# Kernel tuning notes

Measured on AMD Instinct MI355X. Metric: run time of the kernel, lower is better.

The kernel has to match this reference:

```python
import jax, jax.numpy as jnp
import numpy as np

NODE_IN = 163   # sum of X_MAP category sizes
HIDDEN = 64
N_NODES = 100_000
N_EDGES = 1_600_000
N_GRAPHS = 1024
SLOPE = 0.01    # F.leaky_relu default negative slope


def _linear_init(key, fan_in, fan_out):
    kw, kb = jax.random.split(key)
    bound = 1.0 / np.sqrt(fan_in)
    W = jax.random.uniform(kw, (fan_in, fan_out), jnp.float32, -bound, bound)
    b = jax.random.uniform(kb, (fan_out,), jnp.float32, -bound, bound)
    return W, b


def setup_inputs() -> dict:
    key = jax.random.key(0)
    ks = jax.random.split(key, 8)
    x = jax.random.normal(ks[0], (N_NODES, NODE_IN), jnp.float32)
    edge_index = jax.random.randint(ks[1], (2, N_EDGES), 0, N_NODES)
    batch = jnp.sort(jax.random.randint(ks[2], (N_NODES,), 0, N_GRAPHS))
    W0, b0 = _linear_init(ks[3], NODE_IN, HIDDEN)
    W1, b1 = _linear_init(ks[4], HIDDEN, HIDDEN)
    W2, b2 = _linear_init(ks[5], HIDDEN, HIDDEN)
    fc1_W, fc1_b = _linear_init(ks[6], HIDDEN, HIDDEN)
    fc2_W, fc2_b = _linear_init(ks[7], HIDDEN, 1)
    return {"x": x, "edge_index": edge_index, "batch": batch,
            "W0": W0, "b0": b0, "W1": W1, "b1": b1, "W2": W2, "b2": b2,
            "fc1_W": fc1_W, "fc1_b": fc1_b, "fc2_W": fc2_W, "fc2_b": fc2_b}


def reference(x, edge_index, batch, W0, b0, W1, b1, W2, b2, fc1_W, fc1_b, fc2_W, fc2_b):
    src, dst = edge_index[0], edge_index[1]
    # GCN symmetric norm with self-loops: deg[i] = 1 + in-degree(i)
    deg = jax.ops.segment_sum(jnp.ones(N_EDGES, x.dtype), dst, N_NODES) + 1.0
    dis = jax.lax.rsqrt(deg)               # deg^{-1/2}
    edge_norm = dis[src] * dis[dst]        # [E]
    self_norm = dis * dis                  # deg^{-1} for self-loop term

    def gcn_conv(h, W, b):
        h = h @ W                                   # [N, hidden]
        msg = h[src] * edge_norm[:, None]           # gather + scale, [E, hidden]
        agg = jax.ops.segment_sum(msg, dst, N_NODES)
        agg = agg + h * self_norm[:, None]          # self-loop contribution
        return agg + b

    h = x
    for W, b in ((W0, b0), (W1, b1), (W2, b2)):
        h = jax.nn.leaky_relu(gcn_conv(h, W, b), SLOPE)
        # dropout: eval mode (identity)

    # global_mean_pool over batch segments
    counts = jax.ops.segment_sum(jnp.ones(N_NODES, h.dtype), batch, N_GRAPHS)
    pooled = jax.ops.segment_sum(h, batch, N_GRAPHS) / jnp.maximum(counts, 1.0)[:, None]

    out = jax.nn.leaky_relu(pooled @ fc1_W + fc1_b, SLOPE)
    return (out @ fc2_W + fc2_b).squeeze(-1)       # [N_GRAPHS]
```

## Files before the change

kernel.cpp:

```cpp
#include <hip/hip_runtime.h>

#define NN 100000
#define NE 1600000
#define NG 1024
#define NODE_IN 163
#define SLOPE 0.01f
#define NBUK 391
#define BUKSH 8
#define EPB 8192
#define NBLK ((NE + EPB - 1) / EPB)

typedef short s16x8 __attribute__((ext_vector_type(8)));
typedef float f32x4 __attribute__((ext_vector_type(4)));

__device__ __forceinline__ unsigned short bf16_rne(float x) {
  unsigned u = __float_as_uint(x);
  return (unsigned short)((u + 0x7FFFu + ((u >> 16) & 1u)) >> 16);
}
__device__ __forceinline__ float bf16_f32(unsigned short h) {
  return __uint_as_float(((unsigned)h) << 16);
}

__global__ void k_hist(const int* __restrict__ dst, int* __restrict__ bh, int E) {
  __shared__ int h[NBUK];
  for (int i = threadIdx.x; i < NBUK; i += 256) h[i] = 0;
  __syncthreads();
  int beg = blockIdx.x * EPB, end = min(E, beg + EPB);
  for (int e = beg + threadIdx.x; e < end; e += 256) atomicAdd(&h[dst[e] >> BUKSH], 1);
  __syncthreads();
  for (int i = threadIdx.x; i < NBUK; i += 256) bh[blockIdx.x * NBUK + i] = h[i];
}

__global__ void k_bucket_scan(int* __restrict__ bh, int* __restrict__ btot) {
  __shared__ int s[256];
  int bucket = blockIdx.x, tid = threadIdx.x;
  int v = (tid < NBLK) ? bh[tid * NBUK + bucket] : 0;
  s[tid] = v;
  __syncthreads();
  for (int off = 1; off < 256; off <<= 1) {
    int t = (tid >= off) ? s[tid - off] : 0;
    __syncthreads();
    s[tid] += t;
    __syncthreads();
  }
  if (tid < NBLK) bh[tid * NBUK + bucket] = s[tid] - v;
  if (tid == 255) btot[bucket] = s[255];
}

__global__ void k_btot_scan(const int* __restrict__ btot, int* __restrict__ boffs, int E) {
  __shared__ int s[512];
  int tid = threadIdx.x;
  int v = (tid < NBUK) ? btot[tid] : 0;
  s[tid] = v;
  __syncthreads();
  for (int off = 1; off < 512; off <<= 1) {
    int t = (tid >= off) ? s[tid - off] : 0;
    __syncthreads();
    s[tid] += t;
    __syncthreads();
  }
  if (tid < NBUK) boffs[tid] = s[tid] - v;
  if (tid == 0) boffs[NBUK] = E;
}

__global__ void k_scatter(const int* __restrict__ src, const int* __restrict__ dst,
                          const int* __restrict__ bh, const int* __restrict__ boffs,
                          unsigned* __restrict__ bedge, int E) {
  __shared__ int cur[NBUK];
  for (int i = threadIdx.x; i < NBUK; i += 256)
    cur[i] = boffs[i] + bh[blockIdx.x * NBUK + i];
  __syncthreads();
  int beg = blockIdx.x * EPB, end = min(E, beg + EPB);
  for (int e = beg + threadIdx.x; e < end; e += 256) {
    int d = dst[e];
    int pos = atomicAdd(&cur[d >> BUKSH], 1);
    bedge[pos] = (unsigned)src[e] | ((unsigned)(d & 255) << 17);
  }
}

__global__ void k_b2csr(const unsigned* __restrict__ bedge, const int* __restrict__ boffs,
                        int* __restrict__ offs, float* __restrict__ dis,
                        int* __restrict__ csr, int N) {
  __shared__ int lcnt[256];
  __shared__ int s[256];
  __shared__ int lcur[256];
  int b = blockIdx.x, tid = threadIdx.x;
  int beg = boffs[b], end = boffs[b + 1];
  lcnt[tid] = 0;
  __syncthreads();
  for (int e = beg + tid; e < end; e += 256) atomicAdd(&lcnt[bedge[e] >> 17], 1);
  __syncthreads();
  int v = lcnt[tid];
  s[tid] = v;
  __syncthreads();
  for (int off = 1; off < 256; off <<= 1) {
    int t = (tid >= off) ? s[tid - off] : 0;
    __syncthreads();
    s[tid] += t;
    __syncthreads();
  }
  int o = s[tid] - v;
  int node = (b << BUKSH) + tid;
  if (node <= N) offs[node] = beg + o;
  if (node < N) dis[node] = rsqrtf((float)(v + 1));
  lcur[tid] = o;
  __syncthreads();
  for (int e = beg + tid; e < end; e += 256) {
    unsigned w = bedge[e];
    int p = atomicAdd(&lcur[w >> 17], 1);
    csr[beg + p] = (int)(w & 0x1FFFFu);
  }
}

__global__ void k_wsplit(const float* __restrict__ W, short* __restrict__ hi,
                         short* __restrict__ lo, int K, int KP) {
  int idx = blockIdx.x * 256 + threadIdx.x;
  if (idx >= 64 * KP) return;
  int c = idx / KP, kk = idx - c * KP;
  float v = (kk < K) ? W[(size_t)kk * 64 + c] : 0.f;
  unsigned short h = bf16_rne(v);
  hi[idx] = (short)h;
  lo[idx] = (short)bf16_rne(v - bf16_f32(h));
}

template<int K, int KP>
__launch_bounds__(256)
__global__ void k_gemm(const float* __restrict__ X, const short* __restrict__ Whi,
                       const short* __restrict__ Wlo, const float* __restrict__ disv,
                       unsigned short* __restrict__ Y, int N) {
  constexpr int KC = KP / 32;
  constexpr int PA = 40;
  constexpr int PB = 40;
  __shared__ __align__(16) short sAh[2][128 * PA];
  __shared__ __align__(16) short sAl[2][128 * PA];
  __shared__ __align__(16) short sBh[2][64 * PB];
  __shared__ __align__(16) short sBl[2][64 * PB];

  const int tid = threadIdx.x;
  const int lane = tid & 63, wv = tid >> 6;
  const int l15 = lane & 15, l4 = lane >> 4;
  const int gbase = blockIdx.x << 7;

  const int arow = tid >> 1, akh = (tid & 1) << 4;
  int grow = gbase + arow;
  if (K != KP) grow = min(grow, N - 1);
  const float* xr = X + (size_t)grow * K;
  const int bcol = tid >> 2, bk8 = (tid & 3) << 3;

  float4 ra0, ra1, ra2, ra3;
  s16x8 rbh, rbl;

  auto loadA = [&](int c) {
    if (K != KP && c == KC - 1) {
      ra0 = ra1 = ra2 = ra3 = make_float4(0.f, 0.f, 0.f, 0.f);
      if (akh == 0) { ra0.x = xr[160]; ra0.y = xr[161]; ra0.z = xr[162]; }
    } else {
      const float* p = xr + c * 32 + akh;
      ra0 = *(const float4*)(p);
      ra1 = *(const float4*)(p + 4);
      ra2 = *(const float4*)(p + 8);
      ra3 = *(const float4*)(p + 12);
    }
  };
  auto loadB = [&](int c) {
    const size_t o = (size_t)bcol * KP + c * 32 + bk8;
    rbh = *(const s16x8*)(Whi + o);
    rbl = *(const s16x8*)(Wlo + o);
  };
  auto writeLDS = [&](int b) {
    short hb[16], lb[16];
    float v[16] = {ra0.x, ra0.y, ra0.z, ra0.w, ra1.x, ra1.y, ra1.z, ra1.w,
                   ra2.x, ra2.y, ra2.z, ra2.w, ra3.x, ra3.y, ra3.z, ra3.w};
    #pragma unroll
    for (int j = 0; j < 16; ++j) {
      unsigned short h = bf16_rne(v[j]);
      hb[j] = (short)h;
      lb[j] = (short)bf16_rne(v[j] - bf16_f32(h));
    }
    short* ah = sAh[b] + arow * PA + akh;
    *(s16x8*)(ah) = *(const s16x8*)(hb);
    *(s16x8*)(ah + 8) = *(const s16x8*)(hb + 8);
    short* al = sAl[b] + arow * PA + akh;
    *(s16x8*)(al) = *(const s16x8*)(lb);
    *(s16x8*)(al + 8) = *(const s16x8*)(lb + 8);
    *(s16x8*)(sBh[b] + bcol * PB + bk8) = rbh;
    *(s16x8*)(sBl[b] + bcol * PB + bk8) = rbl;
  };

  f32x4 acc[2][4];
  #pragma unroll
  for (int rt = 0; rt < 2; ++rt)
    #pragma unroll
    for (int ct = 0; ct < 4; ++ct) acc[rt][ct] = (f32x4){0.f, 0.f, 0.f, 0.f};

  loadA(0); loadB(0); writeLDS(0);
  __syncthreads();

  #pragma unroll 1
  for (int c = 0; c < KC; ++c) {
    if (c + 1 < KC) { loadA(c + 1); loadB(c + 1); }
    const int b = c & 1;
    const int aoff0 = (wv * 32 + l15) * PA + l4 * 8;
    const int aoff1 = aoff0 + 16 * PA;
    s16x8 a0h = *(const s16x8*)(sAh[b] + aoff0);
    s16x8 a0l = *(const s16x8*)(sAl[b] + aoff0);
    s16x8 a1h = *(const s16x8*)(sAh[b] + aoff1);
    s16x8 a1l = *(const s16x8*)(sAl[b] + aoff1);
    #pragma unroll
    for (int ct = 0; ct < 4; ++ct) {
      const int boff = (ct * 16 + l15) * PB + l4 * 8;
      s16x8 bh = *(const s16x8*)(sBh[b] + boff);
      s16x8 bl = *(const s16x8*)(sBl[b] + boff);
      acc[0][ct] = __builtin_amdgcn_mfma_f32_16x16x32_bf16(a0h, bh, acc[0][ct], 0, 0, 0);
      acc[0][ct] = __builtin_amdgcn_mfma_f32_16x16x32_bf16(a0l, bh, acc[0][ct], 0, 0, 0);
      acc[0][ct] = __builtin_amdgcn_mfma_f32_16x16x32_bf16(a0h, bl, acc[0][ct], 0, 0, 0);
      acc[1][ct] = __builtin_amdgcn_mfma_f32_16x16x32_bf16(a1h, bh, acc[1][ct], 0, 0, 0);
      acc[1][ct] = __builtin_amdgcn_mfma_f32_16x16x32_bf16(a1l, bh, acc[1][ct], 0, 0, 0);
      acc[1][ct] = __builtin_amdgcn_mfma_f32_16x16x32_bf16(a1h, bl, acc[1][ct], 0, 0, 0);
    }
    if (c + 1 < KC) { writeLDS((c + 1) & 1); __syncthreads(); }
  }

  const int rb = gbase + wv * 32;
  #pragma unroll
  for (int rt = 0; rt < 2; ++rt) {
    #pragma unroll
    for (int j = 0; j < 4; ++j) {
      int row = rb + rt * 16 + l4 * 4 + j;
      if (row < N) {
        float d = disv[row];
        unsigned short* yp = Y + ((size_t)row << 6) + l15;
        yp[0]  = bf16_rne(acc[rt][0][j] * d);
        yp[16] = bf16_rne(acc[rt][1][j] * d);
        yp[32] = bf16_rne(acc[rt][2][j] * d);
        yp[48] = bf16_rne(acc[rt][3][j] * d);
      }
    }
  }
}

__launch_bounds__(256)
__global__ void k_agg(const unsigned short* __restrict__ G, const int* __restrict__ offs,
                      const int* __restrict__ csr, const float* __restrict__ dis,
                      const float* __restrict__ bias, float* __restrict__ H, int N) {
  int node = blockIdx.x * 4 + (threadIdx.x >> 6);
  if (node >= N) return;
  const int lane = threadIdx.x & 63;
  const int g = lane >> 4, p = lane & 15;
  const ushort4* G4 = (const ushort4*)G;
  int beg = offs[node], end = offs[node + 1];
  float ax = 0.f, ay = 0.f, az = 0.f, aw = 0.f;
  int e = beg + g;
  for (; e + 12 < end; e += 16) {
    int s0 = csr[e], s1 = csr[e + 4], s2 = csr[e + 8], s3 = csr[e + 12];
    ushort4 v0 = G4[(size_t)s0 * 16 + p];
    ushort4 v1 = G4[(size_t)s1 * 16 + p];
    ushort4 v2 = G4[(size_t)s2 * 16 + p];
    ushort4 v3 = G4[(size_t)s3 * 16 + p];
    ax += bf16_f32(v0.x) + bf16_f32(v1.x) + bf16_f32(v2.x) + bf16_f32(v3.x);
    ay += bf16_f32(v0.y) + bf16_f32(v1.y) + bf16_f32(v2.y) + bf16_f32(v3.y);
    az += bf16_f32(v0.z) + bf16_f32(v1.z) + bf16_f32(v2.z) + bf16_f32(v3.z);
    aw += bf16_f32(v0.w) + bf16_f32(v1.w) + bf16_f32(v2.w) + bf16_f32(v3.w);
  }
  for (; e < end; e += 4) {
    int s = csr[e];
    ushort4 v = G4[(size_t)s * 16 + p];
    ax += bf16_f32(v.x); ay += bf16_f32(v.y);
    az += bf16_f32(v.z); aw += bf16_f32(v.w);
  }
  #pragma unroll
  for (int off = 16; off < 64; off <<= 1) {
    ax += __shfl_xor(ax, off, 64);
    ay += __shfl_xor(ay, off, 64);
    az += __shfl_xor(az, off, 64);
    aw += __shfl_xor(aw, off, 64);
  }
  if (g == 0) {
    ushort4 sv = G4[(size_t)node * 16 + p];
    float d = dis[node];
    float4 bq = ((const float4*)bias)[p];
    float ox = (ax + bf16_f32(sv.x)) * d + bq.x;
    float oy = (ay + bf16_f32(sv.y)) * d + bq.y;
    float oz = (az + bf16_f32(sv.z)) * d + bq.z;
    float ow = (aw + bf16_f32(sv.w)) * d + bq.w;
    ox = (ox > 0.f) ? ox : SLOPE * ox;
    oy = (oy > 0.f) ? oy : SLOPE * oy;
    oz = (oz > 0.f) ? oz : SLOPE * oz;
    ow = (ow > 0.f) ? ow : SLOPE * ow;
    ((float4*)(H + ((size_t)node << 6)))[p] = make_float4(ox, oy, oz, ow);
  }
}

__launch_bounds__(64)
__global__ void k_pool(const float* __restrict__ H, const int* __restrict__ batch,
                       const float* __restrict__ f1W, const float* __restrict__ f1b,
                       const float* __restrict__ f2W, const float* __restrict__ f2b,
                       float* __restrict__ out, int N) {
  int g = blockIdx.x;
  int lane = threadIdx.x;
  int lo = 0, hi = N;
  while (lo < hi) { int m = (lo + hi) >> 1; if (batch[m] < g) lo = m + 1; else hi = m; }
  int beg = lo;
  hi = N;
  while (lo < hi) { int m = (lo + hi) >> 1; if (batch[m] < g + 1) lo = m + 1; else hi = m; }
  int end = lo;
  float acc = 0.f;
  for (int r = beg; r < end; ++r) acc += H[(size_t)r * 64 + lane];
  float c = (float)(end - beg);
  acc /= (c < 1.f ? 1.f : c);
  __shared__ float p[64];
  p[lane] = acc;
  __syncthreads();
  float q = f1b[lane];
  #pragma unroll
  for (int k = 0; k < 64; ++k) q += p[k] * f1W[k * 64 + lane];
  q = (q > 0.f) ? q : SLOPE * q;
  float v = q * f2W[lane];
  #pragma unroll
  for (int off = 32; off > 0; off >>= 1) v += __shfl_down(v, off, 64);
  if (lane == 0) out[g] = v + f2b[0];
}

extern "C" void kernel_launch(void* const* d_in, const int* in_sizes, int n_in,
                              void* d_out, int out_size, void* d_ws, size_t ws_size,
                              hipStream_t stream) {
  const float* x    = (const float*)d_in[0];
  const int*  eidx  = (const int*)d_in[1];
  const int*  batch = (const int*)d_in[2];
  const float* W0 = (const float*)d_in[3];
  const float* b0 = (const float*)d_in[4];
  const float* W1 = (const float*)d_in[5];
  const float* b1 = (const float*)d_in[6];
  const float* W2 = (const float*)d_in[7];
  const float* b2 = (const float*)d_in[8];
  const float* f1W = (const float*)d_in[9];
  const float* f1b = (const float*)d_in[10];
  const float* f2W = (const float*)d_in[11];
  const float* f2b = (const float*)d_in[12];
  float* out = (float*)d_out;

  const int N = NN, E = NE;
  const int* src  = eidx;
  const int* dstp = eidx + E;

  const size_t NPAD = 100096;
  char* w = (char*)d_ws;
  float* H     = (float*)w; w += NPAD * 64 * 4;
  unsigned short* G = (unsigned short*)w; w += NPAD * 64 * 2;
  int*   csr   = (int*)w;   w += (size_t)E * 4;
  int*   offs  = (int*)w;   w += (size_t)(N + 4) * 4;
  float* dis   = (float*)w; w += (size_t)N * 4;
  int*   bh    = (int*)w;   w += (size_t)NBLK * NBUK * 4;
  int*   btot  = (int*)w;   w += (NBUK + 1) * 4;
  int*   boffs = (int*)w;   w += (NBUK + 4) * 4;
  short* wt0h  = (short*)w; w += 64 * 192 * 2;
  short* wt0l  = (short*)w; w += 64 * 192 * 2;
  short* wt1h  = (short*)w; w += 64 * 64 * 2;
  short* wt1l  = (short*)w; w += 64 * 64 * 2;
  short* wt2h  = (short*)w; w += 64 * 64 * 2;
  short* wt2l  = (short*)w; w += 64 * 64 * 2;
  unsigned* bedge = (unsigned*)H;

  k_wsplit<<<48, 256, 0, stream>>>(W0, wt0h, wt0l, NODE_IN, 192);
  k_wsplit<<<16, 256, 0, stream>>>(W1, wt1h, wt1l, 64, 64);
  k_wsplit<<<16, 256, 0, stream>>>(W2, wt2h, wt2l, 64, 64);

  k_hist<<<NBLK, 256, 0, stream>>>(dstp, bh, E);
  k_bucket_scan<<<NBUK, 256, 0, stream>>>(bh, btot);
  k_btot_scan<<<1, 512, 0, stream>>>(btot, boffs, E);
  k_scatter<<<NBLK, 256, 0, stream>>>(src, dstp, bh, boffs, bedge, E);
  k_b2csr<<<NBUK, 256, 0, stream>>>(bedge, boffs, offs, dis, csr, N);

  const int NTB = (N + 127) / 128;
  k_gemm<NODE_IN, 192><<<NTB, 256, 0, stream>>>(x, wt0h, wt0l, dis, G, N);
  k_agg<<<(N + 3) / 4, 256, 0, stream>>>(G, offs, csr, dis, b0, H, N);
  k_gemm<64, 64><<<NTB, 256, 0, stream>>>(H, wt1h, wt1l, dis, G, N);
  k_agg<<<(N + 3) / 4, 256, 0, stream>>>(G, offs, csr, dis, b1, H, N);
  k_gemm<64, 64><<<NTB, 256, 0, stream>>>(H, wt2h, wt2l, dis, G, N);
  k_agg<<<(N + 3) / 4, 256, 0, stream>>>(G, offs, csr, dis, b2, H, N);
  k_pool<<<NG, 64, 0, stream>>>(H, batch, f1W, f1b, f2W, f2b, out, N);
}
```

Measured before the change: 308.6 us.

## Split gathered features into four column planes to shrink gather working set

The GEMM now writes its bf16 output as four planes of 16 columns each instead of 64-column rows. The aggregation kernel launches four times as many blocks, ordered plane by plane, so each block gathers only 32-byte rows from one plane. The intent is for each pass's random-gather working set (about 3.2 MB per plane) to stay cache-resident. The cost is re-reading the CSR indices and offsets four times and issuing narrower, less efficient loads.

```diff
diff --git a/kernel.cpp b/kernel.cpp
--- a/kernel.cpp
+++ b/kernel.cpp
@@ -9,6 +9,9 @@
 #define BUKSH 8
 #define EPB 8192
 #define NBLK ((NE + EPB - 1) / EPB)
+#define NPADC 100096
+#define PLANE ((size_t)NPADC * 16)
+#define BPP 25000
 
 typedef short s16x8 __attribute__((ext_vector_type(8)));
 typedef float f32x4 __attribute__((ext_vector_type(4)));
@@ -229,11 +232,11 @@
       int row = rb + rt * 16 + l4 * 4 + j;
       if (row < N) {
         float d = disv[row];
-        unsigned short* yp = Y + ((size_t)row << 6) + l15;
-        yp[0]  = bf16_rne(acc[rt][0][j] * d);
-        yp[16] = bf16_rne(acc[rt][1][j] * d);
-        yp[32] = bf16_rne(acc[rt][2][j] * d);
-        yp[48] = bf16_rne(acc[rt][3][j] * d);
+        size_t ro = ((size_t)row << 4) + l15;
+        Y[0 * PLANE + ro] = bf16_rne(acc[rt][0][j] * d);
+        Y[1 * PLANE + ro] = bf16_rne(acc[rt][1][j] * d);
+        Y[2 * PLANE + ro] = bf16_rne(acc[rt][2][j] * d);
+        Y[3 * PLANE + ro] = bf16_rne(acc[rt][3][j] * d);
       }
     }
   }
@@ -243,51 +246,44 @@
 __global__ void k_agg(const unsigned short* __restrict__ G, const int* __restrict__ offs,
                       const int* __restrict__ csr, const float* __restrict__ dis,
                       const float* __restrict__ bias, float* __restrict__ H, int N) {
-  int node = blockIdx.x * 4 + (threadIdx.x >> 6);
-  if (node >= N) return;
+  const int bid = blockIdx.x;
+  const int q = bid / BPP;
+  const int node = (bid - q * BPP) * 4 + (threadIdx.x >> 6);
   const int lane = threadIdx.x & 63;
-  const int g = lane >> 4, p = lane & 15;
-  const ushort4* G4 = (const ushort4*)G;
-  int beg = offs[node], end = offs[node + 1];
-  float ax = 0.f, ay = 0.f, az = 0.f, aw = 0.f;
+  const int g = lane >> 3, p = lane & 7;
+  const unsigned short* Gq = G + (size_t)q * PLANE;
+  const int beg = offs[node], end = offs[node + 1];
+  float ax = 0.f, ay = 0.f;
   int e = beg + g;
-  for (; e + 12 < end; e += 16) {
-    int s0 = csr[e], s1 = csr[e + 4], s2 = csr[e + 8], s3 = csr[e + 12];
-    ushort4 v0 = G4[(size_t)s0 * 16 + p];
-    ushort4 v1 = G4[(size_t)s1 * 16 + p];
-    ushort4 v2 = G4[(size_t)s2 * 16 + p];
-    ushort4 v3 = G4[(size_t)s3 * 16 + p];
+  for (; e + 24 < end; e += 32) {
+    int s0 = csr[e], s1 = csr[e + 8], s2 = csr[e + 16], s3 = csr[e + 24];
+    ushort2 v0 = *(const ushort2*)(Gq + ((size_t)s0 << 4) + (p << 1));
+    ushort2 v1 = *(const ushort2*)(Gq + ((size_t)s1 << 4) + (p << 1));
+    ushort2 v2 = *(const ushort2*)(Gq + ((size_t)s2 << 4) + (p << 1));
+    ushort2 v3 = *(const ushort2*)(Gq + ((size_t)s3 << 4) + (p << 1));
     ax += bf16_f32(v0.x) + bf16_f32(v1.x) + bf16_f32(v2.x) + bf16_f32(v3.x);
     ay += bf16_f32(v0.y) + bf16_f32(v1.y) + bf16_f32(v2.y) + bf16_f32(v3.y);
-    az += bf16_f32(v0.z) + bf16_f32(v1.z) + bf16_f32(v2.z) + bf16_f32(v3.z);
-    aw += bf16_f32(v0.w) + bf16_f32(v1.w) + bf16_f32(v2.w) + bf16_f32(v3.w);
-  }
-  for (; e < end; e += 4) {
+  }
+  for (; e < end; e += 8) {
     int s = csr[e];
-    ushort4 v = G4[(size_t)s * 16 + p];
-    ax += bf16_f32(v.x); ay += bf16_f32(v.y);
-    az += bf16_f32(v.z); aw += bf16_f32(v.w);
-  }
-  #pragma unroll
-  for (int off = 16; off < 64; off <<= 1) {
+    ushort2 v = *(const ushort2*)(Gq + ((size_t)s << 4) + (p << 1));
+    ax += bf16_f32(v.x);
+    ay += bf16_f32(v.y);
+  }
+  #pragma unroll
+  for (int off = 8; off < 64; off <<= 1) {
     ax += __shfl_xor(ax, off, 64);
     ay += __shfl_xor(ay, off, 64);
-    az += __shfl_xor(az, off, 64);
-    aw += __shfl_xor(aw, off, 64);
   }
   if (g == 0) {
-    ushort4 sv = G4[(size_t)node * 16 + p];
+    ushort2 sv = *(const ushort2*)(Gq + ((size_t)node << 4) + (p << 1));
     float d = dis[node];
-    float4 bq = ((const float4*)bias)[p];
+    float2 bq = ((const float2*)(bias + (q << 4)))[p];
     float ox = (ax + bf16_f32(sv.x)) * d + bq.x;
     float oy = (ay + bf16_f32(sv.y)) * d + bq.y;
-    float oz = (az + bf16_f32(sv.z)) * d + bq.z;
-    float ow = (aw + bf16_f32(sv.w)) * d + bq.w;
     ox = (ox > 0.f) ? ox : SLOPE * ox;
     oy = (oy > 0.f) ? oy : SLOPE * oy;
-    oz = (oz > 0.f) ? oz : SLOPE * oz;
-    ow = (ow > 0.f) ? ow : SLOPE * ow;
-    ((float4*)(H + ((size_t)node << 6)))[p] = make_float4(ox, oy, oz, ow);
+    *(float2*)(H + ((size_t)node << 6) + (q << 4) + (p << 1)) = make_float2(ox, oy);
   }
 }
 
@@ -343,10 +339,9 @@
   const int* src  = eidx;
   const int* dstp = eidx + E;
 
-  const size_t NPAD = 100096;
   char* w = (char*)d_ws;
-  float* H     = (float*)w; w += NPAD * 64 * 4;
-  unsigned short* G = (unsigned short*)w; w += NPAD * 64 * 2;
+  float* H     = (float*)w; w += (size_t)NPADC * 64 * 4;
+  unsigned short* G = (unsigned short*)w; w += (size_t)NPADC * 64 * 2;
   int*   csr   = (int*)w;   w += (size_t)E * 4;
   int*   offs  = (int*)w;   w += (size_t)(N + 4) * 4;
   float* dis   = (float*)w; w += (size_t)N * 4;
@@ -373,10 +368,10 @@
 
   const int NTB = (N + 127) / 128;
   k_gemm<NODE_IN, 192><<<NTB, 256, 0, stream>>>(x, wt0h, wt0l, dis, G, N);
-  k_agg<<<(N + 3) / 4, 256, 0, stream>>>(G, offs, csr, dis, b0, H, N);
+  k_agg<<<4 * BPP, 256, 0, stream>>>(G, offs, csr, dis, b0, H, N);
   k_gemm<64, 64><<<NTB, 256, 0, stream>>>(H, wt1h, wt1l, dis, G, N);
-  k_agg<<<(N + 3) / 4, 256, 0, stream>>>(G, offs, csr, dis, b1, H, N);
+  k_agg<<<4 * BPP, 256, 0, stream>>>(G, offs, csr, dis, b1, H, N);
   k_gemm<64, 64><<<NTB, 256, 0, stream>>>(H, wt2h, wt2l, dis, G, N);
-  k_agg<<<(N + 3) / 4, 256, 0, stream>>>(G, offs, csr, dis, b2, H, N);
+  k_agg<<<4 * BPP, 256, 0, stream>>>(G, offs, csr, dis, b2, H, N);
   k_pool<<<NG, 64, 0, stream>>>(H, batch, f1W, f1b, f2W, f2b, out, N);
 }
```

Result: slower. 563.0 us (+82.5%).
